# Kernel optimization log

Measured on AMD Instinct MI355X. Metric: run time of the kernel, lower is better.

## Reference

```python
import jax, jax.numpy as jnp
import numpy as np

ALPHA = 0.5
NEG_INF_DIAG = 1e6


def setup_inputs() -> dict:
    key = jax.random.key(0)
    k1, k2, k3, k4 = jax.random.split(key, 4)
    B, Nq, Ns, D = 64, 32, 1024, 128
    return {
        "query_single": jax.random.normal(k1, (B, D), dtype=jnp.float32),
        "doc_single": jax.random.normal(k2, (B, D), dtype=jnp.float32),
        "query_multi": jax.random.normal(k3, (B, Nq, D), dtype=jnp.float32),
        "doc_multi": jax.random.normal(k4, (B, Ns, D), dtype=jnp.float32),
    }


def _single_vector_loss(q, d):
    # q, d: (B, D) -> in-batch softmax cross-entropy with diagonal targets
    scores = jnp.einsum("bd,cd->bc", q, d)  # (B, B)
    logp = jax.nn.log_softmax(scores, axis=-1)
    return -jnp.mean(jnp.diagonal(logp))


def _multi_vector_loss(q, d):
    # q: (B, Nq, D), d: (B, Ns, D)
    # MaxSim: max over doc tokens, sum over query tokens
    sim = jnp.einsum("bnd,csd->bcns", q, d)  # (B, B, Nq, Ns) -- large intermediate
    scores = jnp.sum(jnp.max(sim, axis=3), axis=2)  # (B, B)
    pos = jnp.diagonal(scores)  # (B,)
    B = scores.shape[0]
    neg = jnp.max(scores - jnp.eye(B, dtype=scores.dtype) * NEG_INF_DIAG, axis=1)
    return jnp.mean(jax.nn.softplus(neg - pos))


def reference(query_single, doc_single, query_multi, doc_multi):
    sv_loss = _single_vector_loss(query_single, doc_single)
    mv_loss = _multi_vector_loss(query_multi, doc_multi)
    total = ALPHA * sv_loss + (1.0 - ALPHA) * mv_loss
    return sv_loss, mv_loss, total
```

## Files before the change

kernel.cpp:

```cpp
#include <hip/hip_runtime.h>


typedef __attribute__((ext_vector_type(8))) short short8;
typedef __attribute__((ext_vector_type(4))) float f32x4;

static __device__ __forceinline__ unsigned short f2bf(float f) {
  unsigned int u = __float_as_uint(f);
  u += 0x7fffu + ((u >> 16) & 1u);
  return (unsigned short)(u >> 16);
}

static __device__ __forceinline__ void g2l16(const void* g, void* l) {
  __builtin_amdgcn_global_load_lds(
      (const __attribute__((address_space(1))) unsigned int*)g,
      (__attribute__((address_space(3))) unsigned int*)l, 16, 0, 0);
}

__global__ void convert_kernel(const float* __restrict__ qm,
                               const float* __restrict__ dm,
                               unsigned char* __restrict__ dmb,
                               unsigned short* __restrict__ qmb) {
  const int NDM = 1048576;
  const int NT = NDM + 32768;
  for (int g = blockIdx.x * 256 + threadIdx.x; g < NT;
       g += gridDim.x * 256) {
    const float* src;
    unsigned char* dst;
    if (g < NDM) {
      const int c = g >> 14;
      const int r = g & 16383;
      const int s = r >> 4;
      const int kc = r & 15;
      src = dm + ((size_t)c * 131072 + (size_t)s * 128 + kc * 8);
      dst = dmb + ((size_t)c * 262144 + s * 256 +
                   ((kc * 16) ^ ((s & 7) << 4)));
    } else {
      const int gg = g - NDM;
      const int row = gg >> 4;
      const int kc = gg & 15;
      src = qm + (size_t)row * 128 + kc * 8;
      dst = (unsigned char*)(qmb + (size_t)row * 128 + kc * 8);
    }
    const float4 a = *(const float4*)src;
    const float4 b = *(const float4*)(src + 4);
    short8 w;
    w[0] = (short)f2bf(a.x); w[1] = (short)f2bf(a.y);
    w[2] = (short)f2bf(a.z); w[3] = (short)f2bf(a.w);
    w[4] = (short)f2bf(b.x); w[5] = (short)f2bf(b.y);
    w[6] = (short)f2bf(b.z); w[7] = (short)f2bf(b.w);
    *(short8*)dst = w;
  }
}

__global__ __launch_bounds__(256, 2) void mv_kernel(
    const unsigned short* __restrict__ qmb,
    const unsigned char* __restrict__ dmb,
    const float* __restrict__ qs, const float* __restrict__ ds,
    float* __restrict__ scores, float* __restrict__ svp) {
  __shared__ __align__(16) unsigned char smem[33792];

  const int tid = threadIdx.x;
  const int ln = tid & 63;
  const int wv = tid >> 6;

  if (blockIdx.y == 64) {
    const int rb = blockIdx.x;
    float* dl = (float*)smem;
    for (int i = tid; i < 8192; i += 256)
      dl[(i >> 7) * 129 + (i & 127)] = ds[i];
    __syncthreads();
    const int cc = ln;
    for (int rr = 0; rr < 2; ++rr) {
      const int row = rb * 8 + wv * 2 + rr;
      const float* q = qs + (size_t)row * 128;
      float acc = 0.f;
#pragma unroll
      for (int k = 0; k < 128; ++k) acc += q[k] * dl[cc * 129 + k];
      float m = acc;
      for (int d = 1; d < 64; d <<= 1) m = fmaxf(m, __shfl_xor(m, d));
      float e = expf(acc - m);
      float ssum = e;
      for (int d = 1; d < 64; d <<= 1) ssum += __shfl_xor(ssum, d);
      const float lp = acc - m - logf(ssum);
      const float diag = __shfl(lp, row);
      if (ln == 0) svp[row] = -diag;
    }
    return;
  }

  const int c = blockIdx.y;
  const int rb = blockIdx.x;
  const int lrow = ln & 15;
  const int lkg = ln >> 4;

  short8 qf[4][4];
#pragma unroll
  for (int rt = 0; rt < 4; ++rt) {
    const int row = rb * 256 + wv * 64 + rt * 16 + lrow;
    const unsigned short* qp = qmb + (size_t)row * 128 + lkg * 8;
#pragma unroll
    for (int kk = 0; kk < 4; ++kk)
      qf[rt][kk] = *(const short8*)(qp + kk * 32);
  }

  f32x4 maxv[4];
#pragma unroll
  for (int rt = 0; rt < 4; ++rt)
#pragma unroll
    for (int r = 0; r < 4; ++r) maxv[rt][r] = -3.0e38f;

  const unsigned char* dbase = dmb + (size_t)c * 262144;
  float* rowmax = (float*)(smem + 32768);

#pragma unroll
  for (int i = 0; i < 4; ++i) {
    const int chunk = wv * 4 + i;
    g2l16(dbase + chunk * 1024 + ln * 16, smem + chunk * 1024);
  }
  __syncthreads();

  for (int t = 0; t < 16; ++t) {
    const unsigned char* cur = smem + (t & 1) * 16384;
    if (t < 15) {
      unsigned char* nxt = smem + ((t + 1) & 1) * 16384;
      const unsigned char* gsrc = dbase + (t + 1) * 16384;
#pragma unroll
      for (int i = 0; i < 4; ++i) {
        const int chunk = wv * 4 + i;
        g2l16(gsrc + chunk * 1024 + ln * 16, nxt + chunk * 1024);
      }
    }
#pragma unroll
    for (int cc = 0; cc < 4; ++cc) {
      const int s = cc * 16 + lrow;
      const unsigned char* bp = cur + s * 256;
      const int swz = (s & 7) << 4;
      short8 df[4];
#pragma unroll
      for (int kk = 0; kk < 4; ++kk)
        df[kk] = *(const short8*)(bp + ((kk * 64 + lkg * 16) ^ swz));
#pragma unroll
      for (int rt = 0; rt < 4; ++rt) {
        f32x4 a = {0.f, 0.f, 0.f, 0.f};
#pragma unroll
        for (int kk = 0; kk < 4; ++kk)
          a = __builtin_amdgcn_mfma_f32_16x16x32_bf16(qf[rt][kk], df[kk], a,
                                                      0, 0, 0);
#pragma unroll
        for (int r = 0; r < 4; ++r) maxv[rt][r] = fmaxf(maxv[rt][r], a[r]);
      }
    }
    __syncthreads();
  }

#pragma unroll
  for (int rt = 0; rt < 4; ++rt)
#pragma unroll
    for (int r = 0; r < 4; ++r) {
      float v = maxv[rt][r];
      v = fmaxf(v, __shfl_xor(v, 1));
      v = fmaxf(v, __shfl_xor(v, 2));
      v = fmaxf(v, __shfl_xor(v, 4));
      v = fmaxf(v, __shfl_xor(v, 8));
      if (lrow == 0) rowmax[wv * 64 + rt * 16 + lkg * 4 + r] = v;
    }
  __syncthreads();

  {
    float v = rowmax[tid];
    v += __shfl_xor(v, 1);
    v += __shfl_xor(v, 2);
    v += __shfl_xor(v, 4);
    v += __shfl_xor(v, 8);
    v += __shfl_xor(v, 16);
    if ((tid & 31) == 0) {
      const int b = rb * 8 + (tid >> 5);
      scores[b * 64 + c] = v;
    }
  }
}

__global__ void final_kernel(const float* __restrict__ scores,
                             const float* __restrict__ svp,
                             float* __restrict__ out) {
  const int b = threadIdx.x;
  float sv = svp[b];
  for (int d = 1; d < 64; d <<= 1) sv += __shfl_xor(sv, d);
  sv *= (1.0f / 64.0f);

  const float pos = scores[b * 64 + b];
  float neg = -3.0e38f;
  for (int c = 0; c < 64; ++c) {
    float v = scores[b * 64 + c] - (c == b ? 1.0e6f : 0.0f);
    neg = fmaxf(neg, v);
  }
  const float t = neg - pos;
  float sp = fmaxf(t, 0.f) + log1pf(expf(-fabsf(t)));
  for (int d = 1; d < 64; d <<= 1) sp += __shfl_xor(sp, d);
  if (b == 0) {
    const float mvl = sp / 64.0f;
    out[0] = sv;
    out[1] = mvl;
    out[2] = 0.5f * sv + 0.5f * mvl;
  }
}

__global__ void sv_kernel_fb(const float* __restrict__ qs,
                             const float* __restrict__ ds,
                             float* __restrict__ out_sv) {
  __shared__ float sc[64][64];
  const int tid = threadIdx.x;
  for (int p = tid; p < 4096; p += 256) {
    const int b = p >> 6, c = p & 63;
    const float4* qa = (const float4*)(qs + b * 128);
    const float4* da = (const float4*)(ds + c * 128);
    float acc = 0.f;
#pragma unroll
    for (int i = 0; i < 32; ++i) {
      const float4 x = qa[i], y = da[i];
      acc += x.x * y.x + x.y * y.y + x.z * y.z + x.w * y.w;
    }
    sc[b][c] = acc;
  }
  __syncthreads();
  if (tid < 64) {
    float m = -3.0e38f;
    for (int c = 0; c < 64; ++c) m = fmaxf(m, sc[tid][c]);
    float s = 0.f;
    for (int c = 0; c < 64; ++c) s += expf(sc[tid][c] - m);
    float lp = sc[tid][tid] - (m + logf(s));
    for (int d = 1; d < 64; d <<= 1) lp += __shfl_xor(lp, d);
    if (tid == 0) *out_sv = -lp / 64.0f;
  }
}

__global__ __launch_bounds__(256, 4) void mv_gemm_fb(
    const float* __restrict__ qm, const float* __restrict__ dm,
    float* __restrict__ scores) {
  __shared__ unsigned char dtb[64 * 256];
  __shared__ float rowmax[128];
  const int c = blockIdx.y;
  const int rb = blockIdx.x;
  const int tid = threadIdx.x;
  const int ln = tid & 63;
  const int wv = tid >> 6;
  const int lrow = ln & 15;
  const int lkg = ln >> 4;
  short8 qf[2][4];
#pragma unroll
  for (int rt = 0; rt < 2; ++rt) {
    const int row = rb * 128 + wv * 32 + rt * 16 + lrow;
    const float* qp = qm + (size_t)row * 128 + lkg * 8;
#pragma unroll
    for (int kk = 0; kk < 4; ++kk) {
      const float4 a = *(const float4*)(qp + kk * 32);
      const float4 b = *(const float4*)(qp + kk * 32 + 4);
      short8 f;
      f[0] = (short)f2bf(a.x); f[1] = (short)f2bf(a.y);
      f[2] = (short)f2bf(a.z); f[3] = (short)f2bf(a.w);
      f[4] = (short)f2bf(b.x); f[5] = (short)f2bf(b.y);
      f[6] = (short)f2bf(b.z); f[7] = (short)f2bf(b.w);
      qf[rt][kk] = f;
    }
  }
  f32x4 maxv[2];
#pragma unroll
  for (int rt = 0; rt < 2; ++rt)
#pragma unroll
    for (int r = 0; r < 4; ++r) maxv[rt][r] = -3.0e38f;
  const float* dbase = dm + (size_t)c * 1024 * 128;
  for (int t = 0; t < 16; ++t) {
    __syncthreads();
#pragma unroll
    for (int i = 0; i < 4; ++i) {
      const int ch = tid + i * 256;
      const int s = ch >> 4;
      const int kc = ch & 15;
      const float* p = dbase + (size_t)(t * 64 + s) * 128 + kc * 8;
      const float4 a = *(const float4*)p;
      const float4 b = *(const float4*)(p + 4);
      short8 w;
      w[0] = (short)f2bf(a.x); w[1] = (short)f2bf(a.y);
      w[2] = (short)f2bf(a.z); w[3] = (short)f2bf(a.w);
      w[4] = (short)f2bf(b.x); w[5] = (short)f2bf(b.y);
      w[6] = (short)f2bf(b.z); w[7] = (short)f2bf(b.w);
      *(short8*)(dtb + s * 256 + ((kc * 16) ^ ((s & 7) << 4))) = w;
    }
    __syncthreads();
#pragma unroll
    for (int cc = 0; cc < 4; ++cc) {
      const int s = cc * 16 + lrow;
      short8 df[4];
#pragma unroll
      for (int kk = 0; kk < 4; ++kk)
        df[kk] = *(const short8*)(dtb + s * 256 +
                                  ((kk * 64 + lkg * 16) ^ ((s & 7) << 4)));
#pragma unroll
      for (int rt = 0; rt < 2; ++rt) {
        f32x4 acc = {0.f, 0.f, 0.f, 0.f};
#pragma unroll
        for (int kk = 0; kk < 4; ++kk)
          acc = __builtin_amdgcn_mfma_f32_16x16x32_bf16(qf[rt][kk], df[kk],
                                                        acc, 0, 0, 0);
#pragma unroll
        for (int r = 0; r < 4; ++r) maxv[rt][r] = fmaxf(maxv[rt][r], acc[r]);
      }
    }
  }
#pragma unroll
  for (int rt = 0; rt < 2; ++rt)
#pragma unroll
    for (int r = 0; r < 4; ++r) {
      float v = maxv[rt][r];
      v = fmaxf(v, __shfl_xor(v, 1));
      v = fmaxf(v, __shfl_xor(v, 2));
      v = fmaxf(v, __shfl_xor(v, 4));
      v = fmaxf(v, __shfl_xor(v, 8));
      maxv[rt][r] = v;
    }
  if (lrow == 0) {
#pragma unroll
    for (int rt = 0; rt < 2; ++rt)
#pragma unroll
      for (int r = 0; r < 4; ++r)
        rowmax[wv * 32 + rt * 16 + lkg * 4 + r] = maxv[rt][r];
  }
  __syncthreads();
  if (tid < 128) {
    float v = rowmax[tid];
    v += __shfl_xor(v, 1);
    v += __shfl_xor(v, 2);
    v += __shfl_xor(v, 4);
    v += __shfl_xor(v, 8);
    v += __shfl_xor(v, 16);
    if ((tid & 31) == 0) scores[(rb * 4 + (tid >> 5)) * 64 + c] = v;
  }
}

__global__ void final_fb(const float* __restrict__ scores,
                         const float* __restrict__ sv_ptr,
                         float* __restrict__ out) {
  const int b = threadIdx.x;
  const float pos = scores[b * 64 + b];
  float neg = -3.0e38f;
  for (int c = 0; c < 64; ++c) {
    float v = scores[b * 64 + c] - (c == b ? 1.0e6f : 0.0f);
    neg = fmaxf(neg, v);
  }
  const float t = neg - pos;
  float sp = fmaxf(t, 0.f) + log1pf(expf(-fabsf(t)));
  for (int d = 1; d < 64; d <<= 1) sp += __shfl_xor(sp, d);
  if (b == 0) {
    const float mvl = sp / 64.0f;
    const float sv = *sv_ptr;
    out[0] = sv;
    out[1] = mvl;
    out[2] = 0.5f * sv + 0.5f * mvl;
  }
}

extern "C" void kernel_launch(void* const* d_in, const int* in_sizes, int n_in,
                              void* d_out, int out_size, void* d_ws,
                              size_t ws_size, hipStream_t stream) {
  const float* qs = (const float*)d_in[0];
  const float* ds = (const float*)d_in[1];
  const float* qm = (const float*)d_in[2];
  const float* dm = (const float*)d_in[3];
  float* out = (float*)d_out;

  const size_t NEED = 16777216u + 524288u + 16384u + 256u;
  if (ws_size >= NEED) {
    unsigned char* dmb = (unsigned char*)d_ws;
    unsigned short* qmb = (unsigned short*)(dmb + 16777216u);
    float* scores = (float*)(dmb + 16777216u + 524288u);
    float* svp = scores + 4096;
    convert_kernel<<<2048, 256, 0, stream>>>(qm, dm, dmb, qmb);
    mv_kernel<<<dim3(8, 65), 256, 0, stream>>>(qmb, dmb, qs, ds, scores, svp);
    final_kernel<<<1, 64, 0, stream>>>(scores, svp, out);
  } else {
    float* scores = (float*)d_ws;
    float* sv = scores + 4096;
    sv_kernel_fb<<<1, 256, 0, stream>>>(qs, ds, sv);
    mv_gemm_fb<<<dim3(16, 64), 256, 0, stream>>>(qm, dm, scores);
    final_fb<<<1, 64, 0, stream>>>(scores, sv, out);
  }
}
```

Baseline: 51.43 us.

## Split doc tokens across two workgroups and add a max/sum reduce kernel

The MaxSim kernel now splits each document's 1024 tokens into two halves handled by separate workgroups, doubling the grid to 1024 GEMM workgroups plus 8 single-vector ones on a 1D grid. Block ids are remapped with an XCD-style interleave and the occupancy hint is raised to 4 waves per SIMD. Per-row partial maxima go to a new workspace buffer, and a new reduce kernel combines the two halves with max and sums over query tokens. The convert kernel drops its grid-stride loop for one element per thread, also with interleaved block mapping. This exposes more parallelism across the CUs but costs an extra kernel launch and a round trip of the partials through global memory.

Result: slower. 67.00 us (+30.3%).

```diff
diff --git a/kernel.cpp b/kernel.cpp
--- a/kernel.cpp
+++ b/kernel.cpp
@@ -21,50 +21,50 @@
                                unsigned char* __restrict__ dmb,
                                unsigned short* __restrict__ qmb) {
   const int NDM = 1048576;
-  const int NT = NDM + 32768;
-  for (int g = blockIdx.x * 256 + threadIdx.x; g < NT;
-       g += gridDim.x * 256) {
-    const float* src;
-    unsigned char* dst;
-    if (g < NDM) {
-      const int c = g >> 14;
-      const int r = g & 16383;
-      const int s = r >> 4;
-      const int kc = r & 15;
-      src = dm + ((size_t)c * 131072 + (size_t)s * 128 + kc * 8);
-      dst = dmb + ((size_t)c * 262144 + s * 256 +
-                   ((kc * 16) ^ ((s & 7) << 4)));
-    } else {
-      const int gg = g - NDM;
-      const int row = gg >> 4;
-      const int kc = gg & 15;
-      src = qm + (size_t)row * 128 + kc * 8;
-      dst = (unsigned char*)(qmb + (size_t)row * 128 + kc * 8);
-    }
-    const float4 a = *(const float4*)src;
-    const float4 b = *(const float4*)(src + 4);
-    short8 w;
-    w[0] = (short)f2bf(a.x); w[1] = (short)f2bf(a.y);
-    w[2] = (short)f2bf(a.z); w[3] = (short)f2bf(a.w);
-    w[4] = (short)f2bf(b.x); w[5] = (short)f2bf(b.y);
-    w[6] = (short)f2bf(b.z); w[7] = (short)f2bf(b.w);
-    *(short8*)dst = w;
-  }
-}
-
-__global__ __launch_bounds__(256, 2) void mv_kernel(
+  const int j = blockIdx.x;
+  const int rbid = (j & 7) * 528 + (j >> 3);
+  const int g = rbid * 256 + threadIdx.x;
+  const float* src;
+  unsigned char* dst;
+  if (g < NDM) {
+    const int c = g >> 14;
+    const int r = g & 16383;
+    const int s = r >> 4;
+    const int kc = r & 15;
+    src = dm + ((size_t)c * 131072 + (size_t)s * 128 + kc * 8);
+    dst = dmb + ((size_t)c * 262144 + s * 256 +
+                 ((kc * 16) ^ ((s & 7) << 4)));
+  } else {
+    const int gg = g - NDM;
+    const int row = gg >> 4;
+    const int kc = gg & 15;
+    src = qm + (size_t)row * 128 + kc * 8;
+    dst = (unsigned char*)(qmb + (size_t)row * 128 + kc * 8);
+  }
+  const float4 a = *(const float4*)src;
+  const float4 b = *(const float4*)(src + 4);
+  short8 w;
+  w[0] = (short)f2bf(a.x); w[1] = (short)f2bf(a.y);
+  w[2] = (short)f2bf(a.z); w[3] = (short)f2bf(a.w);
+  w[4] = (short)f2bf(b.x); w[5] = (short)f2bf(b.y);
+  w[6] = (short)f2bf(b.z); w[7] = (short)f2bf(b.w);
+  *(short8*)dst = w;
+}
+
+__global__ __launch_bounds__(256, 4) void mv_kernel(
     const unsigned short* __restrict__ qmb,
     const unsigned char* __restrict__ dmb,
     const float* __restrict__ qs, const float* __restrict__ ds,
-    float* __restrict__ scores, float* __restrict__ svp) {
+    float* __restrict__ part, float* __restrict__ svp) {
   __shared__ __align__(16) unsigned char smem[33792];
 
   const int tid = threadIdx.x;
   const int ln = tid & 63;
   const int wv = tid >> 6;
-
-  if (blockIdx.y == 64) {
-    const int rb = blockIdx.x;
+  const int wgid = blockIdx.x;
+
+  if (wgid >= 1024) {
+    const int rb = wgid - 1024;
     float* dl = (float*)smem;
     for (int i = tid; i < 8192; i += 256)
       dl[(i >> 7) * 129 + (i & 127)] = ds[i];
@@ -88,8 +88,12 @@
     return;
   }
 
-  const int c = blockIdx.y;
-  const int rb = blockIdx.x;
+  const int rid = (wgid & 7) * 128 + (wgid >> 3);
+  const int c = rid >> 4;
+  const int rr4 = rid & 15;
+  const int rb = rr4 >> 1;
+  const int sc = rr4 & 1;
+
   const int lrow = ln & 15;
   const int lkg = ln >> 4;
 
@@ -109,7 +113,7 @@
 #pragma unroll
     for (int r = 0; r < 4; ++r) maxv[rt][r] = -3.0e38f;
 
-  const unsigned char* dbase = dmb + (size_t)c * 262144;
+  const unsigned char* dbase = dmb + (size_t)c * 262144 + (size_t)sc * 131072;
   float* rowmax = (float*)(smem + 32768);
 
 #pragma unroll
@@ -119,9 +123,9 @@
   }
   __syncthreads();
 
-  for (int t = 0; t < 16; ++t) {
+  for (int t = 0; t < 8; ++t) {
     const unsigned char* cur = smem + (t & 1) * 16384;
-    if (t < 15) {
+    if (t < 7) {
       unsigned char* nxt = smem + ((t + 1) & 1) * 16384;
       const unsigned char* gsrc = dbase + (t + 1) * 16384;
 #pragma unroll
@@ -166,18 +170,24 @@
     }
   __syncthreads();
 
-  {
-    float v = rowmax[tid];
-    v += __shfl_xor(v, 1);
-    v += __shfl_xor(v, 2);
-    v += __shfl_xor(v, 4);
-    v += __shfl_xor(v, 8);
-    v += __shfl_xor(v, 16);
-    if ((tid & 31) == 0) {
-      const int b = rb * 8 + (tid >> 5);
-      scores[b * 64 + c] = v;
-    }
-  }
+  part[(size_t)(c * 2 + sc) * 2048 + rb * 256 + tid] = rowmax[tid];
+}
+
+__global__ void reduce_kernel(const float* __restrict__ part,
+                              float* __restrict__ scores) {
+  const int c = blockIdx.x;
+  const int t = threadIdx.x;
+  const float* p0 = part + (size_t)(c * 2 + 0) * 2048;
+  const float* p1 = part + (size_t)(c * 2 + 1) * 2048;
+  float s = 0.f;
+#pragma unroll
+  for (int i = 0; i < 8; ++i) {
+    const int r = t * 8 + i;
+    s += fmaxf(p0[r], p1[r]);
+  }
+  s += __shfl_xor(s, 1);
+  s += __shfl_xor(s, 2);
+  if ((t & 3) == 0) scores[(t >> 2) * 64 + c] = s;
 }
 
 __global__ void final_kernel(const float* __restrict__ scores,
@@ -368,14 +378,16 @@
   const float* dm = (const float*)d_in[3];
   float* out = (float*)d_out;
 
-  const size_t NEED = 16777216u + 524288u + 16384u + 256u;
+  const size_t NEED = 16777216u + 524288u + 1048576u + 16384u + 256u;
   if (ws_size >= NEED) {
     unsigned char* dmb = (unsigned char*)d_ws;
     unsigned short* qmb = (unsigned short*)(dmb + 16777216u);
-    float* scores = (float*)(dmb + 16777216u + 524288u);
+    float* part = (float*)(dmb + 16777216u + 524288u);
+    float* scores = (float*)(dmb + 16777216u + 524288u + 1048576u);
     float* svp = scores + 4096;
-    convert_kernel<<<2048, 256, 0, stream>>>(qm, dm, dmb, qmb);
-    mv_kernel<<<dim3(8, 65), 256, 0, stream>>>(qmb, dmb, qs, ds, scores, svp);
+    convert_kernel<<<4224, 256, 0, stream>>>(qm, dm, dmb, qmb);
+    mv_kernel<<<1032, 256, 0, stream>>>(qmb, dmb, qs, ds, part, svp);
+    reduce_kernel<<<64, 256, 0, stream>>>(part, scores);
     final_kernel<<<1, 64, 0, stream>>>(scores, svp, out);
   } else {
     float* scores = (float*)d_ws;
```
